# Performance work log

Hardware: AMD Instinct MI355X
Metric: run time of the kernel (lower is better)

## Reference

```python
import jax, jax.numpy as jnp
import numpy as np

B, T, LA, L = 4, 32, 32, 512
D, H, C = 2048, 16, 128
KV_DIM = 2048
K = T * LA  # total kv tokens per batch element
EPS = 1e-5


def _ln(x):
    m = jnp.mean(x, axis=-1, keepdims=True)
    v = jnp.var(x, axis=-1, keepdims=True)
    return (x - m) * jax.lax.rsqrt(v + EPS)


def setup_inputs() -> dict:
    key = jax.random.key(0)
    ks = jax.random.split(key, 10)
    s = 1.0 / np.sqrt(D)
    sk = 1.0 / np.sqrt(KV_DIM)
    return {
        "x": jax.random.normal(ks[0], (B, T, LA, KV_DIM), jnp.float32),
        "latents": jax.random.normal(ks[1], (B, L, D), jnp.float32),
        "t_emb": jax.random.normal(ks[2], (B, 3, D), jnp.float32) * 0.02,
        "q_lens": jnp.full((B,), L, dtype=jnp.int32),
        "k_lens": jax.random.randint(ks[3], (B,), K // 2, K + 1).astype(jnp.int32),
        "ln_kv_w": jnp.ones((KV_DIM,), jnp.float32),
        "ln_kv_b": jnp.zeros((KV_DIM,), jnp.float32),
        "ssg": jax.random.normal(ks[4], (1, 3, D), jnp.float32) * s,  # shift_scale_gate param (adaLN=True)
        "Wq": jax.random.normal(ks[5], (D, D), jnp.float32) * s,
        "bq": jnp.zeros((D,), jnp.float32),
        "Wkv": jax.random.normal(ks[6], (KV_DIM, 2 * D), jnp.float32) * sk,
        "bkv": jnp.zeros((2 * D,), jnp.float32),
        "Wo": jax.random.normal(ks[7], (D, D), jnp.float32) * s,
        "bo": jnp.zeros((D,), jnp.float32),
    }


def reference(x, latents, t_emb, q_lens, k_lens, ln_kv_w, ln_kv_b, ssg,
              Wq, bq, Wkv, bkv, Wo, bo):
    # norm_kv (affine LayerNorm over kv_dim)
    xk = _ln(x) * ln_kv_w + ln_kv_b  # (B,T,LA,KV_DIM)
    # AdaLN modulate: shift/scale/gate from t_emb + learned shift_scale_gate
    mod = t_emb + ssg  # (B,3,D)
    shift, scale, gate = mod[:, 0:1], mod[:, 1:2], mod[:, 2:3]  # (B,1,D)
    norm_q = _ln(latents)  # norm_q has no affine when adaLN=True
    lat = norm_q * (1.0 + scale) + shift
    # projections
    q = (lat @ Wq + bq).reshape(B, L, H, C)
    kv = (xk.reshape(B, K, KV_DIM) @ Wkv + bkv)  # (B,K,2D)
    k, v = kv[..., :D], kv[..., D:]
    k = k.reshape(B, K, H, C)
    v = v.reshape(B, K, H, C)
    # varlen attention == per-batch masked attention (keys beyond k_lens masked)
    scores = jnp.einsum("blhc,bkhc->bhlk", q, k) / np.sqrt(C)
    kmask = jnp.arange(K)[None, :] < k_lens[:, None]  # (B,K)
    scores = jnp.where(kmask[:, None, None, :], scores, jnp.finfo(scores.dtype).min)
    attn = jax.nn.softmax(scores, axis=-1)
    out = jnp.einsum("bhlk,bkhc->blhc", attn, v).reshape(B, L, D)
    # queries beyond q_lens are invalid -> zero them (varlen packing semantics)
    qmask = (jnp.arange(L)[None, :] < q_lens[:, None])[..., None]  # (B,L,1)
    out = out * qmask
    return (out @ Wo + bo) * gate
```

## Files before the change

### kernel.cpp

```cpp
#include <hip/hip_runtime.h>

typedef unsigned short u16;
typedef short bf16x8 __attribute__((ext_vector_type(8)));
typedef float f32x4 __attribute__((ext_vector_type(4)));

#define MFMA_BF16(a, b, c) __builtin_amdgcn_mfma_f32_16x16x32_bf16((a), (b), (c), 0, 0, 0)
#define ATT_SCALE 0.08838834764831845f

__device__ __forceinline__ u16 f2bf(float f) {
  union { float f; unsigned int u; } cv;
  cv.f = f;
  unsigned int u = cv.u + 0x7fffu + ((cv.u >> 16) & 1u);
  return (u16)(u >> 16);
}

__global__ __launch_bounds__(256) void prep_kernel(
    const float* __restrict__ x, const float* __restrict__ ln_w,
    const float* __restrict__ ln_b, const float* __restrict__ latents,
    const float* __restrict__ t_emb, const float* __restrict__ ssg,
    const float* __restrict__ Wq, const float* __restrict__ Wo,
    const float* __restrict__ Wkv,
    u16* __restrict__ xk_out, u16* __restrict__ lat_out,
    u16* __restrict__ WqT, u16* __restrict__ WoT, u16* __restrict__ WkvT)
{
  __shared__ float shmem[32 * 33];
  const int blk = blockIdx.x;
  const int tid = threadIdx.x;
  if (blk < 6144) {
    const bool is_x = blk < 4096;
    const int row = is_x ? blk : blk - 4096;
    const float* src = is_x ? (x + (size_t)row * 2048) : (latents + (size_t)row * 2048);
    const float4* xr = (const float4*)src;
    float4 v0 = xr[tid];
    float4 v1 = xr[tid + 256];
    float sum = v0.x + v0.y + v0.z + v0.w + v1.x + v1.y + v1.z + v1.w;
    float sq  = v0.x*v0.x + v0.y*v0.y + v0.z*v0.z + v0.w*v0.w
              + v1.x*v1.x + v1.y*v1.y + v1.z*v1.z + v1.w*v1.w;
    #pragma unroll
    for (int off = 32; off > 0; off >>= 1) {
      sum += __shfl_xor(sum, off);
      sq  += __shfl_xor(sq, off);
    }
    if ((tid & 63) == 0) { shmem[tid >> 6] = sum; shmem[(tid >> 6) + 4] = sq; }
    __syncthreads();
    sum = shmem[0] + shmem[1] + shmem[2] + shmem[3];
    sq  = shmem[4] + shmem[5] + shmem[6] + shmem[7];
    const float mean = sum * (1.0f / 2048.0f);
    const float var  = sq * (1.0f / 2048.0f) - mean * mean;
    const float rstd = rsqrtf(var + 1e-5f);
    if (is_x) {
      const float4* w4 = (const float4*)ln_w;
      const float4* b4 = (const float4*)ln_b;
      ushort4* orow = (ushort4*)(xk_out + (size_t)row * 2048);
      #pragma unroll
      for (int j = 0; j < 2; ++j) {
        const int idx = tid + j * 256;
        const float4 v = j ? v1 : v0;
        const float4 ww = w4[idx];
        const float4 bb = b4[idx];
        ushort4 o;
        o.x = f2bf((v.x - mean) * rstd * ww.x + bb.x);
        o.y = f2bf((v.y - mean) * rstd * ww.y + bb.y);
        o.z = f2bf((v.z - mean) * rstd * ww.z + bb.z);
        o.w = f2bf((v.w - mean) * rstd * ww.w + bb.w);
        orow[idx] = o;
      }
    } else {
      const int bidx = row >> 9;
      const float4* te = (const float4*)(t_emb + (size_t)bidx * 3 * 2048);
      const float4* sg = (const float4*)ssg;
      ushort4* orow = (ushort4*)(lat_out + (size_t)row * 2048);
      #pragma unroll
      for (int j = 0; j < 2; ++j) {
        const int idx = tid + j * 256;
        const float4 v = j ? v1 : v0;
        const float4 t0 = te[idx];
        const float4 t1 = te[512 + idx];
        const float4 s0 = sg[idx];
        const float4 s1 = sg[512 + idx];
        ushort4 o;
        o.x = f2bf(((v.x - mean) * rstd) * (1.0f + t1.x + s1.x) + (t0.x + s0.x));
        o.y = f2bf(((v.y - mean) * rstd) * (1.0f + t1.y + s1.y) + (t0.y + s0.y));
        o.z = f2bf(((v.z - mean) * rstd) * (1.0f + t1.z + s1.z) + (t0.z + s0.z));
        o.w = f2bf(((v.w - mean) * rstd) * (1.0f + t1.w + s1.w) + (t0.w + s0.w));
        orow[idx] = o;
      }
    }
  } else {
    int t = blk - 6144;
    const float* in;
    u16* outp;
    int C, cx, ry;
    if (t < 4096)      { in = Wq;  outp = WqT;  C = 2048; cx = t & 63;  ry = t >> 6; }
    else if (t < 8192) { t -= 4096; in = Wo;  outp = WoT;  C = 2048; cx = t & 63;  ry = t >> 6; }
    else               { t -= 8192; in = Wkv; outp = WkvT; C = 4096; cx = t & 127; ry = t >> 7; }
    float (*tile)[33] = (float(*)[33])shmem;
    const int R = 2048;
    const int c0 = cx * 32;
    const int r0 = ry * 32;
    const int tx = tid & 31;
    const int ty = tid >> 5;
    #pragma unroll
    for (int i = 0; i < 4; ++i)
      tile[ty + i * 8][tx] = in[(size_t)(r0 + ty + i * 8) * C + c0 + tx];
    __syncthreads();
    #pragma unroll
    for (int i = 0; i < 4; ++i)
      outp[(size_t)(c0 + ty + i * 8) * R + r0 + tx] = f2bf(tile[tx][ty + i * 8]);
  }
}

template<int BM>
__global__ __launch_bounds__(256) void gemm_bf16_kernel(
    const u16* __restrict__ A, const u16* __restrict__ BT,
    int Kd, int mode,
    const float* __restrict__ bias,
    u16* __restrict__ out_q, u16* __restrict__ out_k, u16* __restrict__ out_vT,
    float* __restrict__ out_f,
    const float* __restrict__ t_emb, const float* __restrict__ ssg,
    const int* __restrict__ k_lens)
{
  constexpr int TI = BM / 32;
  __shared__ u16 As[2][BM][40];
  __shared__ u16 Bs[2][128][40];
  const int tid  = threadIdx.x;
  const int lane = tid & 63;
  const int wv   = tid >> 6;
  const int wm   = wv & 1, wn = wv >> 1;
  const int quad = lane >> 4, lq = lane & 15;
  const int m0 = blockIdx.y * BM, n0 = blockIdx.x * 128;

  f32x4 acc[TI][4];
  #pragma unroll
  for (int i = 0; i < TI; ++i)
    #pragma unroll
    for (int j = 0; j < 4; ++j)
      acc[i][j] = (f32x4){0.f, 0.f, 0.f, 0.f};

  int kiters = Kd;
  if (mode == 1 && (m0 & 1023) >= k_lens[m0 >> 10]) kiters = 0;

  const int rB  = tid >> 1;
  const int hfB = (tid & 1) * 16;
  const u16* gB = BT + (size_t)(n0 + rB) * Kd + hfB;
  const int rA  = (BM == 128) ? (tid >> 1) : (tid >> 2);
  const int hA  = (BM == 128) ? 0 : ((tid >> 1) & 1);
  const int hfA = (tid & 1) * 16;
  const u16* gA = A + (size_t)(m0 + rA) * Kd + hA * 32 + hfA;

  for (int k0 = 0; k0 < kiters; k0 += 64) {
    uint4 a00, a01, a10, a11;
    a00 = *(const uint4*)(gA + k0);
    a01 = *(const uint4*)(gA + k0 + 8);
    if (BM == 128) {
      a10 = *(const uint4*)(gA + k0 + 32);
      a11 = *(const uint4*)(gA + k0 + 40);
    }
    const uint4 b00 = *(const uint4*)(gB + k0);
    const uint4 b01 = *(const uint4*)(gB + k0 + 8);
    const uint4 b10 = *(const uint4*)(gB + k0 + 32);
    const uint4 b11 = *(const uint4*)(gB + k0 + 40);
    __syncthreads();
    *(uint4*)&As[hA][rA][hfA]     = a00;
    *(uint4*)&As[hA][rA][hfA + 8] = a01;
    if (BM == 128) {
      *(uint4*)&As[1][rA][hfA]     = a10;
      *(uint4*)&As[1][rA][hfA + 8] = a11;
    }
    *(uint4*)&Bs[0][rB][hfB]     = b00;
    *(uint4*)&Bs[0][rB][hfB + 8] = b01;
    *(uint4*)&Bs[1][rB][hfB]     = b10;
    *(uint4*)&Bs[1][rB][hfB + 8] = b11;
    __syncthreads();
    #pragma unroll
    for (int kk = 0; kk < 2; ++kk) {
      bf16x8 av[TI], bv[4];
      #pragma unroll
      for (int i = 0; i < TI; ++i)
        av[i] = *(const bf16x8*)&As[kk][wm * (BM / 2) + i * 16 + lq][quad * 8];
      #pragma unroll
      for (int j = 0; j < 4; ++j)
        bv[j] = *(const bf16x8*)&Bs[kk][wn * 64 + j * 16 + lq][quad * 8];
      #pragma unroll
      for (int i = 0; i < TI; ++i)
        #pragma unroll
        for (int j = 0; j < 4; ++j)
          acc[i][j] = MFMA_BF16(av[i], bv[j], acc[i][j]);
    }
  }

  #pragma unroll
  for (int i = 0; i < TI; ++i) {
    const int mlb = m0 + wm * (BM / 2) + i * 16 + quad * 4;
    #pragma unroll
    for (int j = 0; j < 4; ++j) {
      const int n = n0 + wn * 64 + j * 16 + lq;
      const float bs = bias[n];
      if (mode == 0) {
        const int h = n >> 7, c = n & 127;
        #pragma unroll
        for (int rr = 0; rr < 4; ++rr) {
          const int m = mlb + rr;
          const int bb = m >> 9, l = m & 511;
          out_q[((size_t)(bb * 16 + h) * 512 + l) * 128 + c] =
              f2bf((acc[i][j][rr] + bs) * ATT_SCALE);
        }
      } else if (mode == 1) {
        if (n < 2048) {
          const int h = n >> 7, c = n & 127;
          #pragma unroll
          for (int rr = 0; rr < 4; ++rr) {
            const int m = mlb + rr;
            const int bb = m >> 10, kk = m & 1023;
            out_k[((size_t)(bb * 16 + h) * 1024 + kk) * 128 + c] = f2bf(acc[i][j][rr] + bs);
          }
        } else {
          const int n2 = n - 2048;
          const int h = n2 >> 7, c = n2 & 127;
          #pragma unroll
          for (int rr = 0; rr < 4; ++rr) {
            const int m = mlb + rr;
            const int bb = m >> 10, kk = m & 1023;
            out_vT[((size_t)(bb * 16 + h) * 128 + c) * 1024 + kk] = f2bf(acc[i][j][rr] + bs);
          }
        }
      } else {
        #pragma unroll
        for (int rr = 0; rr < 4; ++rr) {
          const int m = mlb + rr;
          const int bb = m >> 9;
          const float g = t_emb[((size_t)bb * 3 + 2) * 2048 + n] + ssg[2 * 2048 + n];
          out_f[(size_t)m * 2048 + n] = (acc[i][j][rr] + bs) * g;
        }
      }
    }
  }
}

__global__ __launch_bounds__(256) void attn_kernel(
    const u16* __restrict__ qb, const u16* __restrict__ kb,
    const u16* __restrict__ vT, const int* __restrict__ k_lens,
    const int* __restrict__ q_lens, u16* __restrict__ ao)
{
  __shared__ u16 Ks[64][132];
  __shared__ u16 Vs[128][68];
  __shared__ u16 Ps[64][68];
  const int tid  = threadIdx.x;
  const int w    = tid >> 6;
  const int lane = tid & 63;
  const int quad = lane >> 4, lq = lane & 15;
  const int bh = blockIdx.y;
  const int b  = bh >> 4;
  const int l0 = blockIdx.x * 64;
  const int kl = k_lens[b];
  const int ql = q_lens[b];

  bf16x8 qf[4];
  {
    const u16* qp = qb + ((size_t)bh * 512 + l0 + w * 16 + lq) * 128 + quad * 8;
    #pragma unroll
    for (int ks = 0; ks < 4; ++ks)
      qf[ks] = *(const bf16x8*)(qp + ks * 32);
  }

  const int krow = tid >> 4;
  const int kcol = tid & 15;
  const u16* kg = kb + ((size_t)bh * 1024 + krow) * 128 + kcol * 8;
  const int vrow = tid >> 3;
  const int vcol = tid & 7;
  const u16* vg = vT + (size_t)bh * 128 * 1024 + (size_t)vrow * 1024 + vcol * 8;

  f32x4 o[8];
  #pragma unroll
  for (int j = 0; j < 8; ++j) o[j] = (f32x4){0.f, 0.f, 0.f, 0.f};
  float mrun[4], lrun[4];
  #pragma unroll
  for (int rr = 0; rr < 4; ++rr) { mrun[rr] = -__builtin_inff(); lrun[rr] = 0.f; }

  const int nkt = (kl + 63) >> 6;
  for (int kt = 0; kt < nkt; ++kt) {
    const int k0 = kt * 64;
    uint4 kd[4], vd[4];
    #pragma unroll
    for (int p = 0; p < 4; ++p)
      kd[p] = *(const uint4*)(kg + (size_t)(k0 + p * 16) * 128);
    #pragma unroll
    for (int p = 0; p < 4; ++p)
      vd[p] = *(const uint4*)(vg + (size_t)p * 32 * 1024 + k0);
    __syncthreads();
    #pragma unroll
    for (int p = 0; p < 4; ++p)
      *(uint4*)&Ks[krow + p * 16][kcol * 8] = kd[p];
    #pragma unroll
    for (int p = 0; p < 4; ++p)
      *(uint4*)&Vs[vrow + p * 32][vcol * 8] = vd[p];
    __syncthreads();

    f32x4 s[4];
    #pragma unroll
    for (int ct = 0; ct < 4; ++ct) {
      s[ct] = (f32x4){0.f, 0.f, 0.f, 0.f};
      #pragma unroll
      for (int ks = 0; ks < 4; ++ks) {
        const bf16x8 kf = *(const bf16x8*)&Ks[ct * 16 + lq][ks * 32 + quad * 8];
        s[ct] = MFMA_BF16(qf[ks], kf, s[ct]);
      }
    }
    #pragma unroll
    for (int ct = 0; ct < 4; ++ct) {
      const bool valid = (k0 + ct * 16 + lq) < kl;
      #pragma unroll
      for (int rr = 0; rr < 4; ++rr)
        s[ct][rr] = valid ? s[ct][rr] : -__builtin_inff();
    }
    float mnew[4], alpha[4], rs[4];
    #pragma unroll
    for (int rr = 0; rr < 4; ++rr) {
      float tm = fmaxf(fmaxf(s[0][rr], s[1][rr]), fmaxf(s[2][rr], s[3][rr]));
      tm = fmaxf(tm, __shfl_xor(tm, 1));
      tm = fmaxf(tm, __shfl_xor(tm, 2));
      tm = fmaxf(tm, __shfl_xor(tm, 4));
      tm = fmaxf(tm, __shfl_xor(tm, 8));
      const float mn = fmaxf(mrun[rr], tm);
      alpha[rr] = __expf(mrun[rr] - mn);
      mrun[rr] = mn;
      mnew[rr] = mn;
      rs[rr] = 0.f;
    }
    #pragma unroll
    for (int ct = 0; ct < 4; ++ct)
      #pragma unroll
      for (int rr = 0; rr < 4; ++rr) {
        const float p = __expf(s[ct][rr] - mnew[rr]);
        s[ct][rr] = p;
        rs[rr] += p;
      }
    #pragma unroll
    for (int rr = 0; rr < 4; ++rr) {
      float t = rs[rr];
      t += __shfl_xor(t, 1);
      t += __shfl_xor(t, 2);
      t += __shfl_xor(t, 4);
      t += __shfl_xor(t, 8);
      lrun[rr] = lrun[rr] * alpha[rr] + t;
    }
    #pragma unroll
    for (int j = 0; j < 8; ++j)
      #pragma unroll
      for (int rr = 0; rr < 4; ++rr)
        o[j][rr] *= alpha[rr];

    #pragma unroll
    for (int ct = 0; ct < 4; ++ct)
      #pragma unroll
      for (int rr = 0; rr < 4; ++rr)
        Ps[w * 16 + quad * 4 + rr][ct * 16 + lq] = f2bf(s[ct][rr]);

    bf16x8 pf[2];
    pf[0] = *(const bf16x8*)&Ps[w * 16 + lq][quad * 8];
    pf[1] = *(const bf16x8*)&Ps[w * 16 + lq][32 + quad * 8];

    #pragma unroll
    for (int j = 0; j < 8; ++j) {
      #pragma unroll
      for (int kk = 0; kk < 2; ++kk) {
        const bf16x8 vf = *(const bf16x8*)&Vs[j * 16 + lq][kk * 32 + quad * 8];
        o[j] = MFMA_BF16(pf[kk], vf, o[j]);
      }
    }
  }

  const int h = bh & 15;
  #pragma unroll
  for (int rr = 0; rr < 4; ++rr) {
    const int row = l0 + w * 16 + quad * 4 + rr;
    const float inv = (row < ql) ? (1.0f / lrun[rr]) : 0.0f;
    u16* op = ao + ((size_t)b * 512 + row) * 2048 + h * 128 + lq;
    #pragma unroll
    for (int j = 0; j < 8; ++j)
      op[j * 16] = f2bf(o[j][rr] * inv);
  }
}

extern "C" void kernel_launch(void* const* d_in, const int* in_sizes, int n_in,
                              void* d_out, int out_size, void* d_ws, size_t ws_size,
                              hipStream_t stream) {
  (void)in_sizes; (void)n_in; (void)out_size; (void)ws_size;
  const float* x       = (const float*)d_in[0];
  const float* latents = (const float*)d_in[1];
  const float* t_emb   = (const float*)d_in[2];
  const int*   q_lens  = (const int*)d_in[3];
  const int*   k_lens  = (const int*)d_in[4];
  const float* ln_w    = (const float*)d_in[5];
  const float* ln_b    = (const float*)d_in[6];
  const float* ssg     = (const float*)d_in[7];
  const float* Wq      = (const float*)d_in[8];
  const float* bq      = (const float*)d_in[9];
  const float* Wkv     = (const float*)d_in[10];
  const float* bkv     = (const float*)d_in[11];
  const float* Wo      = (const float*)d_in[12];
  const float* bo      = (const float*)d_in[13];
  float* out = (float*)d_out;

  u16* ws = (u16*)d_ws;
  const size_t MEG = (size_t)1 << 20;
  u16* WqT  = ws;
  u16* WoT  = ws + 4  * MEG;
  u16* WkvT = ws + 8  * MEG;
  u16* xk   = ws + 16 * MEG;
  u16* lat  = ws + 24 * MEG;
  u16* qb   = ws + 28 * MEG;
  u16* kbuf = ws + 32 * MEG;
  u16* vTb  = ws + 40 * MEG;
  u16* aob  = ws + 48 * MEG;

  prep_kernel<<<dim3(22528), dim3(256), 0, stream>>>(
      x, ln_w, ln_b, latents, t_emb, ssg, Wq, Wo, Wkv,
      xk, lat, WqT, WoT, WkvT);

  gemm_bf16_kernel<64><<<dim3(16, 32), dim3(256), 0, stream>>>(
      lat, WqT, 2048, 0, bq, qb, nullptr, nullptr, nullptr, nullptr, nullptr, k_lens);
  gemm_bf16_kernel<128><<<dim3(32, 32), dim3(256), 0, stream>>>(
      xk, WkvT, 2048, 1, bkv, nullptr, kbuf, vTb, nullptr, nullptr, nullptr, k_lens);

  attn_kernel<<<dim3(8, 64), dim3(256), 0, stream>>>(qb, kbuf, vTb, k_lens, q_lens, aob);

  gemm_bf16_kernel<64><<<dim3(16, 32), dim3(256), 0, stream>>>(
      aob, WoT, 2048, 2, bo, nullptr, nullptr, nullptr, out, t_emb, ssg, k_lens);
}
```

Measured before the change: 417.1 us.

## Load GEMM tiles directly into LDS with global_load_lds and K-step 32

Replaces the register-staged global-to-shared copies in the bf16 GEMM with direct global_load_lds transfers of 16 bytes per lane. The K step drops from 64 to 32 and the LDS tiles become unpadded [rows][32] arrays. The template also gains a BN parameter, set to 128 at every launch. The aim is to cut VGPR pressure and the extra LDS-store instructions. In exchange there are twice as many barrier pairs per K, no overlap between loads and MFMAs, and possible LDS bank conflicts now that the padding is gone.

```diff
diff --git a/kernel.cpp b/kernel.cpp
--- a/kernel.cpp
+++ b/kernel.cpp
@@ -12,6 +12,12 @@
   cv.f = f;
   unsigned int u = cv.u + 0x7fffu + ((cv.u >> 16) & 1u);
   return (u16)(u >> 16);
+}
+
+__device__ __forceinline__ void gload_lds16(const u16* g, u16* l) {
+  __builtin_amdgcn_global_load_lds(
+      (const __attribute__((address_space(1))) unsigned int*)g,
+      (__attribute__((address_space(3))) unsigned int*)l, 16, 0, 0);
 }
 
 __global__ __launch_bounds__(256) void prep_kernel(
@@ -110,7 +116,7 @@
   }
 }
 
-template<int BM>
+template<int BM, int BN>
 __global__ __launch_bounds__(256) void gemm_bf16_kernel(
     const u16* __restrict__ A, const u16* __restrict__ BT,
     int Kd, int mode,
@@ -121,80 +127,64 @@
     const int* __restrict__ k_lens)
 {
   constexpr int TI = BM / 32;
-  __shared__ u16 As[2][BM][40];
-  __shared__ u16 Bs[2][128][40];
+  constexpr int TJ = BN / 32;
+  __shared__ u16 As[BM][32];
+  __shared__ u16 Bs[BN][32];
   const int tid  = threadIdx.x;
   const int lane = tid & 63;
   const int wv   = tid >> 6;
   const int wm   = wv & 1, wn = wv >> 1;
   const int quad = lane >> 4, lq = lane & 15;
-  const int m0 = blockIdx.y * BM, n0 = blockIdx.x * 128;
-
-  f32x4 acc[TI][4];
+  const int m0 = blockIdx.y * BM, n0 = blockIdx.x * BN;
+
+  f32x4 acc[TI][TJ];
   #pragma unroll
   for (int i = 0; i < TI; ++i)
     #pragma unroll
-    for (int j = 0; j < 4; ++j)
+    for (int j = 0; j < TJ; ++j)
       acc[i][j] = (f32x4){0.f, 0.f, 0.f, 0.f};
 
   int kiters = Kd;
   if (mode == 1 && (m0 & 1023) >= k_lens[m0 >> 10]) kiters = 0;
 
-  const int rB  = tid >> 1;
-  const int hfB = (tid & 1) * 16;
-  const u16* gB = BT + (size_t)(n0 + rB) * Kd + hfB;
-  const int rA  = (BM == 128) ? (tid >> 1) : (tid >> 2);
-  const int hA  = (BM == 128) ? 0 : ((tid >> 1) & 1);
-  const int hfA = (tid & 1) * 16;
-  const u16* gA = A + (size_t)(m0 + rA) * Kd + hA * 32 + hfA;
-
-  for (int k0 = 0; k0 < kiters; k0 += 64) {
-    uint4 a00, a01, a10, a11;
-    a00 = *(const uint4*)(gA + k0);
-    a01 = *(const uint4*)(gA + k0 + 8);
-    if (BM == 128) {
-      a10 = *(const uint4*)(gA + k0 + 32);
-      a11 = *(const uint4*)(gA + k0 + 40);
-    }
-    const uint4 b00 = *(const uint4*)(gB + k0);
-    const uint4 b01 = *(const uint4*)(gB + k0 + 8);
-    const uint4 b10 = *(const uint4*)(gB + k0 + 32);
-    const uint4 b11 = *(const uint4*)(gB + k0 + 40);
-    __syncthreads();
-    *(uint4*)&As[hA][rA][hfA]     = a00;
-    *(uint4*)&As[hA][rA][hfA + 8] = a01;
-    if (BM == 128) {
-      *(uint4*)&As[1][rA][hfA]     = a10;
-      *(uint4*)&As[1][rA][hfA + 8] = a11;
-    }
-    *(uint4*)&Bs[0][rB][hfB]     = b00;
-    *(uint4*)&Bs[0][rB][hfB + 8] = b01;
-    *(uint4*)&Bs[1][rB][hfB]     = b10;
-    *(uint4*)&Bs[1][rB][hfB + 8] = b11;
-    __syncthreads();
-    #pragma unroll
-    for (int kk = 0; kk < 2; ++kk) {
-      bf16x8 av[TI], bv[4];
-      #pragma unroll
-      for (int i = 0; i < TI; ++i)
-        av[i] = *(const bf16x8*)&As[kk][wm * (BM / 2) + i * 16 + lq][quad * 8];
-      #pragma unroll
-      for (int j = 0; j < 4; ++j)
-        bv[j] = *(const bf16x8*)&Bs[kk][wn * 64 + j * 16 + lq][quad * 8];
-      #pragma unroll
-      for (int i = 0; i < TI; ++i)
-        #pragma unroll
-        for (int j = 0; j < 4; ++j)
-          acc[i][j] = MFMA_BF16(av[i], bv[j], acc[i][j]);
-    }
+  const int lr = lane >> 2;
+  const int lc = (lane & 3) << 3;
+  const u16* gA = A  + (size_t)(m0 + lr) * Kd + lc;
+  const u16* gB = BT + (size_t)(n0 + lr) * Kd + lc;
+
+  for (int k0 = 0; k0 < kiters; k0 += 32) {
+    __syncthreads();
+    #pragma unroll
+    for (int p = 0; p < BM / 64; ++p) {
+      const int ch = wv + (p << 2);
+      gload_lds16(gA + (size_t)(ch * 16) * Kd + k0, &As[ch * 16][0]);
+    }
+    #pragma unroll
+    for (int p = 0; p < BN / 64; ++p) {
+      const int ch = wv + (p << 2);
+      gload_lds16(gB + (size_t)(ch * 16) * Kd + k0, &Bs[ch * 16][0]);
+    }
+    __syncthreads();
+    bf16x8 av[TI], bv[TJ];
+    #pragma unroll
+    for (int i = 0; i < TI; ++i)
+      av[i] = *(const bf16x8*)&As[wm * (BM / 2) + i * 16 + lq][quad * 8];
+    #pragma unroll
+    for (int j = 0; j < TJ; ++j)
+      bv[j] = *(const bf16x8*)&Bs[wn * (BN / 2) + j * 16 + lq][quad * 8];
+    #pragma unroll
+    for (int i = 0; i < TI; ++i)
+      #pragma unroll
+      for (int j = 0; j < TJ; ++j)
+        acc[i][j] = MFMA_BF16(av[i], bv[j], acc[i][j]);
   }
 
   #pragma unroll
   for (int i = 0; i < TI; ++i) {
     const int mlb = m0 + wm * (BM / 2) + i * 16 + quad * 4;
     #pragma unroll
-    for (int j = 0; j < 4; ++j) {
-      const int n = n0 + wn * 64 + j * 16 + lq;
+    for (int j = 0; j < TJ; ++j) {
+      const int n = n0 + wn * (BN / 2) + j * 16 + lq;
       const float bs = bias[n];
       if (mode == 0) {
         const int h = n >> 7, c = n & 127;
@@ -418,13 +408,13 @@
       x, ln_w, ln_b, latents, t_emb, ssg, Wq, Wo, Wkv,
       xk, lat, WqT, WoT, WkvT);
 
-  gemm_bf16_kernel<64><<<dim3(16, 32), dim3(256), 0, stream>>>(
+  gemm_bf16_kernel<64, 128><<<dim3(16, 32), dim3(256), 0, stream>>>(
       lat, WqT, 2048, 0, bq, qb, nullptr, nullptr, nullptr, nullptr, nullptr, k_lens);
-  gemm_bf16_kernel<128><<<dim3(32, 32), dim3(256), 0, stream>>>(
+  gemm_bf16_kernel<128, 128><<<dim3(32, 32), dim3(256), 0, stream>>>(
       xk, WkvT, 2048, 1, bkv, nullptr, kbuf, vTb, nullptr, nullptr, nullptr, k_lens);
 
   attn_kernel<<<dim3(8, 64), dim3(256), 0, stream>>>(qb, kbuf, vTb, k_lens, q_lens, aob);
 
-  gemm_bf16_kernel<64><<<dim3(16, 32), dim3(256), 0, stream>>>(
+  gemm_bf16_kernel<64, 128><<<dim3(16, 32), dim3(256), 0, stream>>>(
       aob, WoT, 2048, 2, bo, nullptr, nullptr, nullptr, out, t_emb, ssg, k_lens);
 }
```

Result: slower. 434.9 us (+4.3%).
